# Kernel tuning notes

Measured on AMD Instinct MI355X. Metric: run time of the kernel, lower is better.

## Reference

```python
import jax, jax.numpy as jnp
import numpy as np

S = 2048        # q_len == context_length
HID = 4096      # hidden_size
NH = 32         # num_attention_heads
NKV = 8         # num_key_value_heads
HD = HID // NH  # head_dim = 128
THETA = 10000.0


def setup_inputs() -> dict:
    key = jax.random.key(0)
    ks = jax.random.split(key, 5)
    hidden_states = jax.random.normal(ks[0], (1, S, HID), dtype=jnp.float32)
    # 1x1 Conv2d weights == linear weights (out_ch, in_ch)
    wq = jax.random.normal(ks[1], (NH * HD, HID), dtype=jnp.float32) * 0.02
    wk = jax.random.normal(ks[2], (NKV * HD, HID), dtype=jnp.float32) * 0.02
    wv = jax.random.normal(ks[3], (NKV * HD, HID), dtype=jnp.float32) * 0.02
    wo = jax.random.normal(ks[4], (HID, NH * HD), dtype=jnp.float32) * 0.02
    # RoPE tables: rotate() only ever uses the first half_dim of cos/sin,
    # so build (1,1,S,half) directly (equivalent to cat(freqs,freqs) then slice).
    half = HD // 2
    inv_freq = 1.0 / (THETA ** (jnp.arange(0, HD, 2, dtype=jnp.float32) / HD))
    freqs = jnp.outer(jnp.arange(S, dtype=jnp.float32), inv_freq)  # (S, half)
    cos = jnp.cos(freqs)[None, None]  # (1,1,S,half)
    sin = jnp.sin(freqs)[None, None]
    # additive causal mask (1,1,S,S): 0 on/below diagonal, large negative above
    causal_mask = jnp.where(
        jnp.arange(S)[:, None] >= jnp.arange(S)[None, :], 0.0, -1e9
    ).astype(jnp.float32)[None, None]
    return dict(hidden_states=hidden_states, wq=wq, wk=wk, wv=wv, wo=wo,
                cos=cos, sin=sin, causal_mask=causal_mask)


def _rope(x, cos, sin):
    # x: (H, S, D); cos/sin: (1,1,S,D/2)
    half = x.shape[-1] // 2
    x1, x2 = x[..., :half], x[..., half:]
    c, s = cos[0, 0], sin[0, 0]  # (S, half), broadcasts over heads
    return jnp.concatenate([x1 * c - x2 * s, x2 * c + x1 * s], axis=-1)


def reference(hidden_states, wq, wk, wv, wo, cos, sin, causal_mask):
    x = hidden_states[0]               # (S, HID); bsz hard-coded to 1 in source
    seq = x.shape[0]
    # 1x1 conv projections == matmul; channel layout is head-major (h*HD + d)
    q = (x @ wq.T).reshape(seq, NH, HD).transpose(1, 0, 2)    # (NH, S, D)
    k = (x @ wk.T).reshape(seq, NKV, HD).transpose(1, 0, 2)   # (NKV, S, D)
    v = (x @ wv.T).reshape(seq, NKV, HD).transpose(1, 0, 2)   # (NKV, S, D)
    q = _rope(q, cos, sin)
    k = _rope(k, cos, sin)
    # repeat_kv: unsqueeze(1).repeat(n_rep).view -> head idx = rep*NKV + kv == tile
    n_rep = NH // NKV
    k = jnp.tile(k, (n_rep, 1, 1))     # (NH, S, D)
    v = jnp.tile(v, (n_rep, 1, 1))
    scale = 1.0 / np.sqrt(HD).astype(np.float32)
    scores = jnp.einsum('hqd,hkd->hqk', q, k) * scale + causal_mask[0, 0]
    attn = jax.nn.softmax(scores, axis=-1)                    # == ANE_softmax
    out = jnp.einsum('hqk,hkd->hqd', attn, v)                 # (NH, S, D)
    out = out.transpose(1, 0, 2).reshape(seq, NH * HD)        # (S, HID)
    return (out @ wo.T)[None]                                 # (1, S, HID)
```

## Files before the change

### kernel.cpp

```cpp
#include <hip/hip_runtime.h>
#include <hip/hip_bf16.h>

#define S_LEN 2048
#define HID   4096
#define NH    32
#define NKV   8
#define HD    128
#define QKV_N 6144
#define KDIM  4096

typedef __attribute__((ext_vector_type(8))) short short8;
typedef __attribute__((ext_vector_type(4))) float floatx4;
typedef unsigned short ushort;

__device__ __forceinline__ unsigned short f2bu(float f) {
  __hip_bfloat16 b = __float2bfloat16(f);
  return *reinterpret_cast<unsigned short*>(&b);
}
__device__ __forceinline__ void store_c(float* p, float v) { *p = v; }
__device__ __forceinline__ void store_c(__hip_bfloat16* p, float v) { *p = __float2bfloat16(v); }

__device__ __forceinline__ void async_copy16(const void* g, void* l) {
  __builtin_amdgcn_global_load_lds((const __attribute__((address_space(1))) void*)g,
                                   (__attribute__((address_space(3))) void*)l, 16, 0, 0);
}

struct bf16x4 { __hip_bfloat16 a, b, c, d; };
__global__ void cvt_f32_bf16(const float* __restrict__ src, __hip_bfloat16* __restrict__ dst, int n4) {
  int i = blockIdx.x * blockDim.x + threadIdx.x;
  if (i < n4) {
    float4 v = ((const float4*)src)[i];
    bf16x4 o = { __float2bfloat16(v.x), __float2bfloat16(v.y),
                 __float2bfloat16(v.z), __float2bfloat16(v.w) };
    ((bf16x4*)dst)[i] = o;
  }
}

template <typename CT>
__global__ __launch_bounds__(256, 2) void gemm_nt(const __hip_bfloat16* __restrict__ A,
                                                  const __hip_bfloat16* __restrict__ B,
                                                  CT* __restrict__ C, int M, int N, int K) {
  __shared__ __align__(16) ushort As[128 * 64];
  __shared__ __align__(16) ushort Bs[128 * 64];
  const int tid  = threadIdx.x;
  const int bm   = blockIdx.y * 128;
  const int bn   = blockIdx.x * 128;
  const int wave = tid >> 6;
  const int lane = tid & 63;
  const int ww   = (wave >> 1) * 64;
  const int wc   = (wave & 1) * 64;
  const int l15  = lane & 15;
  const int quad = lane >> 4;

  const ushort* Au = (const ushort*)A;
  const ushort* Bu = (const ushort*)B;

  const int rr  = lane >> 3;
  const int cc  = lane & 7;
  const int gch = cc ^ rr;
  const ushort* Ag = Au + (size_t)(bm + wave * 32 + rr) * K + gch * 8;
  const ushort* Bg = Bu + (size_t)(bn + wave * 32 + rr) * K + gch * 8;

  floatx4 acc[4][4] = {};

  for (int k0 = 0; k0 < K; k0 += 64) {
    __syncthreads();
#pragma unroll
    for (int e = 0; e < 4; ++e) {
      async_copy16(Ag + (size_t)(e * 8) * K + k0, &As[(wave * 32 + e * 8) * 64]);
      async_copy16(Bg + (size_t)(e * 8) * K + k0, &Bs[(wave * 32 + e * 8) * 64]);
    }
    __syncthreads();
#pragma unroll
    for (int kd = 0; kd < 2; ++kd) {
      short8 af[4], bf[4];
#pragma unroll
      for (int i = 0; i < 4; ++i) {
        af[i] = *(const short8*)&As[(ww + i * 16 + l15) * 64 + ((kd * 4 + quad) ^ (l15 & 7)) * 8];
        bf[i] = *(const short8*)&Bs[(wc + i * 16 + l15) * 64 + ((kd * 4 + quad) ^ (l15 & 7)) * 8];
      }
#pragma unroll
      for (int mi = 0; mi < 4; ++mi)
#pragma unroll
        for (int ni = 0; ni < 4; ++ni)
          acc[mi][ni] = __builtin_amdgcn_mfma_f32_16x16x32_bf16(af[mi], bf[ni], acc[mi][ni], 0, 0, 0);
    }
  }
#pragma unroll
  for (int mi = 0; mi < 4; ++mi)
#pragma unroll
    for (int ni = 0; ni < 4; ++ni)
#pragma unroll
      for (int r = 0; r < 4; ++r) {
        int row = bm + ww + mi * 16 + quad * 4 + r;
        int col = bn + wc + ni * 16 + l15;
        store_c(&C[(size_t)row * N + col], acc[mi][ni][r]);
      }
}

__global__ void rope_qk(const __hip_bfloat16* __restrict__ QKV,
                        const float* __restrict__ cosp, const float* __restrict__ sinp,
                        __hip_bfloat16* __restrict__ Qh, __hip_bfloat16* __restrict__ Kh) {
  int s = blockIdx.y;
  int col = blockIdx.x * 256 + threadIdx.x;
  if (col >= 5120) return;
  const size_t base = (size_t)s * QKV_N;
  float x = __bfloat162float(QKV[base + col]);
  int dd = col & 127;
  float val;
  if (dd < 64) {
    float xp = __bfloat162float(QKV[base + col + 64]);
    val = x * cosp[s * 64 + dd] - xp * sinp[s * 64 + dd];
  } else {
    int f = dd - 64;
    float xp = __bfloat162float(QKV[base + col - 64]);
    val = x * cosp[s * 64 + f] + xp * sinp[s * 64 + f];
  }
  if (col < HID) {
    int h = col >> 7;
    Qh[((size_t)h * S_LEN + s) * HD + dd] = __float2bfloat16(val * 0.08838834764831845f);
  } else {
    int h = (col - HID) >> 7;
    Kh[((size_t)h * S_LEN + s) * HD + dd] = __float2bfloat16(val);
  }
}

__global__ void v_transpose(const __hip_bfloat16* __restrict__ QKV, __hip_bfloat16* __restrict__ Vt) {
  __shared__ ushort tile[64][130];
  int h = blockIdx.y;
  int s0 = blockIdx.x * 64;
  int t = threadIdx.x;
  const ushort* src = (const ushort*)QKV;
#pragma unroll
  for (int i = 0; i < 32; ++i) {
    int flat = i * 256 + t;
    int r = flat >> 7, c = flat & 127;
    tile[r][c] = src[(size_t)(s0 + r) * QKV_N + 5120 + h * 128 + c];
  }
  __syncthreads();
  ushort* dst = (ushort*)Vt;
#pragma unroll
  for (int i = 0; i < 8; ++i) {
    int g = i * 256 + t;
    int d = g >> 4, j4 = (g & 15) * 4;
    ushort4 o;
    o.x = tile[j4][d]; o.y = tile[j4 + 1][d]; o.z = tile[j4 + 2][d]; o.w = tile[j4 + 3][d];
    *(ushort4*)&dst[((size_t)h * HD + d) * S_LEN + s0 + j4] = o;
  }
}

__global__ __launch_bounds__(256, 2) void attn(const __hip_bfloat16* __restrict__ Qh,
                                               const __hip_bfloat16* __restrict__ Kh,
                                               const __hip_bfloat16* __restrict__ Vt,
                                               __hip_bfloat16* __restrict__ AO) {
  __shared__ __align__(16) ushort Ks[2][64][128];
  __shared__ __align__(16) ushort P[4][32][72];
  const int bi   = blockIdx.x;
  const int head = bi & 31;
  const int slot = (bi >> 5) & 7;
  const int qt   = (bi >= 256) ? (2 * slot) : (15 - 2 * slot);
  const int wave = threadIdx.x >> 6;
  const int lane = threadIdx.x & 63;
  const int l15 = lane & 15, quad = lane >> 4;
  const int q0 = qt * 128 + wave * 32;
  const int hk = head & 7;
  const ushort* Qu = (const ushort*)Qh + (size_t)head * S_LEN * HD;
  const ushort* Ku = (const ushort*)Kh + (size_t)hk * S_LEN * HD;
  const ushort* Vu = (const ushort*)Vt + (size_t)hk * HD * S_LEN;

  const int rr4  = lane >> 4;
  const int cc16 = lane & 15;

  short8 qf[2][4];
#pragma unroll
  for (int mt = 0; mt < 2; ++mt)
#pragma unroll
    for (int kd = 0; kd < 4; ++kd)
      qf[mt][kd] = *(const short8*)(Qu + (size_t)(q0 + mt * 16 + l15) * HD + kd * 32 + quad * 8);

  floatx4 o[2][8] = {};
  float mst[2], lsum[2];
  mst[0] = mst[1] = -1e30f;
  lsum[0] = lsum[1] = 0.f;

  const int nsteps = 2 * (qt + 1);
  const int jendw = q0 + 32;

  auto stage = [&](int b, int j0) {
#pragma unroll
    for (int e = 0; e < 4; ++e) {
      int rt = e * 4 + rr4;
      int gc = cc16 ^ rt;
      async_copy16(Ku + (size_t)(j0 + wave * 16 + rt) * HD + gc * 8,
                   &Ks[b][wave * 16 + e * 4][0]);
    }
  };
  stage(0, 0);

  for (int s = 0; s < nsteps; ++s) {
    const int j0 = s * 64;
    __syncthreads();
    if (s + 1 < nsteps) stage((s + 1) & 1, (s + 1) * 64);
    if (j0 >= jendw) continue;
    const int b = s & 1;

    short8 vf0[8];
#pragma unroll
    for (int t = 0; t < 8; ++t)
      vf0[t] = *(const short8*)(Vu + (size_t)(t * 16 + l15) * S_LEN + j0 + quad * 8);

    floatx4 sc[2][4];
#pragma unroll
    for (int mt = 0; mt < 2; ++mt)
#pragma unroll
      for (int nt = 0; nt < 4; ++nt) sc[mt][nt] = floatx4{0.f, 0.f, 0.f, 0.f};
    __builtin_amdgcn_s_setprio(1);
#pragma unroll
    for (int nt = 0; nt < 4; ++nt) {
      short8 kf[4];
#pragma unroll
      for (int kd = 0; kd < 4; ++kd)
        kf[kd] = *(const short8*)&Ks[b][nt * 16 + l15][((kd * 4 + quad) ^ l15) * 8];
#pragma unroll
      for (int mt = 0; mt < 2; ++mt)
#pragma unroll
        for (int kd = 0; kd < 4; ++kd)
          sc[mt][nt] = __builtin_amdgcn_mfma_f32_16x16x32_bf16(kf[kd], qf[mt][kd], sc[mt][nt], 0, 0, 0);
    }
    __builtin_amdgcn_s_setprio(0);

    const bool domask = (j0 + 64 > q0);
#pragma unroll
    for (int mt = 0; mt < 2; ++mt) {
      const int qrow = q0 + mt * 16 + l15;
      float pv[16];
      float vm = -1e30f;
#pragma unroll
      for (int nt = 0; nt < 4; ++nt)
#pragma unroll
        for (int r = 0; r < 4; ++r) {
          float x = sc[mt][nt][r];
          if (domask && (j0 + nt * 16 + quad * 4 + r > qrow)) x = -1e30f;
          pv[nt * 4 + r] = x;
          vm = fmaxf(vm, x);
        }
      vm = fmaxf(vm, __shfl_xor(vm, 16));
      vm = fmaxf(vm, __shfl_xor(vm, 32));
      if (__any(vm > mst[mt] + 8.0f)) {
        const float mnew = fmaxf(mst[mt], vm);
        const float alpha = __expf(mst[mt] - mnew);
        mst[mt] = mnew;
        lsum[mt] *= alpha;
        float ar[4];
#pragma unroll
        for (int r = 0; r < 4; ++r)
          ar[r] = __shfl(alpha, (lane & 48) | (quad * 4 + r));
#pragma unroll
        for (int t = 0; t < 8; ++t)
#pragma unroll
          for (int r = 0; r < 4; ++r) o[mt][t][r] *= ar[r];
      }
      float ps = 0.f;
      ushort pk[16];
#pragma unroll
      for (int i = 0; i < 16; ++i) {
        float p = __expf(pv[i] - mst[mt]);
        ps += p;
        pk[i] = f2bu(p);
      }
      ps += __shfl_xor(ps, 16);
      ps += __shfl_xor(ps, 32);
      lsum[mt] += ps;
#pragma unroll
      for (int nt = 0; nt < 4; ++nt) {
        ushort4 w;
        w.x = pk[nt * 4 + 0]; w.y = pk[nt * 4 + 1];
        w.z = pk[nt * 4 + 2]; w.w = pk[nt * 4 + 3];
        *(ushort4*)&P[wave][mt * 16 + l15][nt * 16 + quad * 4] = w;
      }
    }

    short8 vf1[8];
#pragma unroll
    for (int t = 0; t < 8; ++t)
      vf1[t] = *(const short8*)(Vu + (size_t)(t * 16 + l15) * S_LEN + j0 + 32 + quad * 8);

    asm volatile("s_waitcnt lgkmcnt(0)" ::: "memory");
    short8 pf[2][2];
#pragma unroll
    for (int mt = 0; mt < 2; ++mt)
#pragma unroll
      for (int hh = 0; hh < 2; ++hh)
        pf[mt][hh] = *(const short8*)&P[wave][mt * 16 + l15][hh * 32 + quad * 8];
    __builtin_amdgcn_s_setprio(1);
#pragma unroll
    for (int t = 0; t < 8; ++t)
#pragma unroll
      for (int mt = 0; mt < 2; ++mt) {
        o[mt][t] = __builtin_amdgcn_mfma_f32_16x16x32_bf16(pf[mt][0], vf0[t], o[mt][t], 0, 0, 0);
        o[mt][t] = __builtin_amdgcn_mfma_f32_16x16x32_bf16(pf[mt][1], vf1[t], o[mt][t], 0, 0, 0);
      }
    __builtin_amdgcn_s_setprio(0);
  }

#pragma unroll
  for (int mt = 0; mt < 2; ++mt) {
    float inv[4];
#pragma unroll
    for (int r = 0; r < 4; ++r)
      inv[r] = 1.0f / __shfl(lsum[mt], (lane & 48) | (quad * 4 + r));
#pragma unroll
    for (int r = 0; r < 4; ++r) {
      const int row = q0 + mt * 16 + quad * 4 + r;
#pragma unroll
      for (int t = 0; t < 8; ++t)
        AO[(size_t)row * HID + head * HD + t * 16 + l15] = __float2bfloat16(o[mt][t][r] * inv[r]);
    }
  }
}

extern "C" void kernel_launch(void* const* d_in, const int* in_sizes, int n_in,
                              void* d_out, int out_size, void* d_ws, size_t ws_size,
                              hipStream_t stream) {
  const float* x    = (const float*)d_in[0];
  const float* wq   = (const float*)d_in[1];
  const float* wk   = (const float*)d_in[2];
  const float* wv   = (const float*)d_in[3];
  const float* wo   = (const float*)d_in[4];
  const float* cosp = (const float*)d_in[5];
  const float* sinp = (const float*)d_in[6];
  float* out = (float*)d_out;

  char* ws = (char*)d_ws;
  size_t off = 0;
  auto alloc = [&](size_t bytes) { char* p = ws + off; off += (bytes + 255) & ~255ull; return p; };
  __hip_bfloat16* Xb   = (__hip_bfloat16*)alloc((size_t)S_LEN * KDIM * 2);
  __hip_bfloat16* Wqkv = (__hip_bfloat16*)alloc((size_t)QKV_N * KDIM * 2);
  __hip_bfloat16* Wob  = (__hip_bfloat16*)alloc((size_t)HID * HID * 2);
  __hip_bfloat16* QKVb = (__hip_bfloat16*)alloc((size_t)S_LEN * QKV_N * 2);
  __hip_bfloat16* Qh   = (__hip_bfloat16*)alloc((size_t)NH * S_LEN * HD * 2);
  __hip_bfloat16* Kh   = (__hip_bfloat16*)alloc((size_t)NKV * S_LEN * HD * 2);
  __hip_bfloat16* Vt   = (__hip_bfloat16*)alloc((size_t)NKV * HD * S_LEN * 2);
  __hip_bfloat16* AO   = (__hip_bfloat16*)alloc((size_t)S_LEN * HID * 2);

  auto cvt = [&](const float* s, __hip_bfloat16* dpt, size_t n) {
    int n4 = (int)(n / 4);
    cvt_f32_bf16<<<dim3((n4 + 255) / 256), dim3(256), 0, stream>>>(s, dpt, n4);
  };
  cvt(x, Xb, (size_t)S_LEN * KDIM);
  cvt(wq, Wqkv, (size_t)HID * KDIM);
  cvt(wk, Wqkv + (size_t)HID * KDIM, (size_t)NKV * HD * KDIM);
  cvt(wv, Wqkv + (size_t)(HID + NKV * HD) * KDIM, (size_t)NKV * HD * KDIM);
  cvt(wo, Wob, (size_t)HID * HID);

  gemm_nt<__hip_bfloat16><<<dim3(QKV_N / 128, S_LEN / 128), dim3(256), 0, stream>>>(
      Xb, Wqkv, QKVb, S_LEN, QKV_N, KDIM);
  rope_qk<<<dim3(20, S_LEN), dim3(256), 0, stream>>>(QKVb, cosp, sinp, Qh, Kh);
  v_transpose<<<dim3(S_LEN / 64, NKV), dim3(256), 0, stream>>>(QKVb, Vt);
  attn<<<dim3(512), dim3(256), 0, stream>>>(Qh, Kh, Vt, AO);
  gemm_nt<float><<<dim3(HID / 128, S_LEN / 128), dim3(256), 0, stream>>>(
      AO, Wob, out, S_LEN, HID, KDIM);
}
```

Measured before the change: 551.7 us.

## Shrink attention q-tile to 64 rows and pair causal tiles per block

Each attention block now handles two 64-row query tiles (a late one and its mirror early one) with 16 rows per wave instead of one 128-row tile with 32 rows per wave. This balances causal work per block, drops the masked wasted K steps, and halves register and LDS use per wave, which may allow higher occupancy. It also chains K staging across the two tiles, defers the lsum reduction to the end, and computes exponentials speculatively before the rescale check. The trade-off is that each loaded K/V tile now feeds half as many query rows, so global and LDS traffic per FLOP increases.

```diff
diff --git a/kernel.cpp b/kernel.cpp
--- a/kernel.cpp
+++ b/kernel.cpp
@@ -154,15 +154,13 @@
                                                const __hip_bfloat16* __restrict__ Vt,
                                                __hip_bfloat16* __restrict__ AO) {
   __shared__ __align__(16) ushort Ks[2][64][128];
-  __shared__ __align__(16) ushort P[4][32][72];
+  __shared__ __align__(16) ushort P[4][16][72];
   const int bi   = blockIdx.x;
   const int head = bi & 31;
-  const int slot = (bi >> 5) & 7;
-  const int qt   = (bi >= 256) ? (2 * slot) : (15 - 2 * slot);
+  const int tp   = bi >> 5;
   const int wave = threadIdx.x >> 6;
   const int lane = threadIdx.x & 63;
   const int l15 = lane & 15, quad = lane >> 4;
-  const int q0 = qt * 128 + wave * 32;
   const int hk = head & 7;
   const ushort* Qu = (const ushort*)Qh + (size_t)head * S_LEN * HD;
   const ushort* Ku = (const ushort*)Kh + (size_t)hk * S_LEN * HD;
@@ -170,21 +168,6 @@
 
   const int rr4  = lane >> 4;
   const int cc16 = lane & 15;
-
-  short8 qf[2][4];
-#pragma unroll
-  for (int mt = 0; mt < 2; ++mt)
-#pragma unroll
-    for (int kd = 0; kd < 4; ++kd)
-      qf[mt][kd] = *(const short8*)(Qu + (size_t)(q0 + mt * 16 + l15) * HD + kd * 32 + quad * 8);
-
-  floatx4 o[2][8] = {};
-  float mst[2], lsum[2];
-  mst[0] = mst[1] = -1e30f;
-  lsum[0] = lsum[1] = 0.f;
-
-  const int nsteps = 2 * (qt + 1);
-  const int jendw = q0 + 32;
 
   auto stage = [&](int b, int j0) {
 #pragma unroll
@@ -195,126 +178,133 @@
                    &Ks[b][wave * 16 + e * 4][0]);
     }
   };
+
+  int gpar = 0;
   stage(0, 0);
 
-  for (int s = 0; s < nsteps; ++s) {
-    const int j0 = s * 64;
-    __syncthreads();
-    if (s + 1 < nsteps) stage((s + 1) & 1, (s + 1) * 64);
-    if (j0 >= jendw) continue;
-    const int b = s & 1;
-
-    short8 vf0[8];
-#pragma unroll
-    for (int t = 0; t < 8; ++t)
-      vf0[t] = *(const short8*)(Vu + (size_t)(t * 16 + l15) * S_LEN + j0 + quad * 8);
-
-    floatx4 sc[2][4];
-#pragma unroll
-    for (int mt = 0; mt < 2; ++mt)
-#pragma unroll
-      for (int nt = 0; nt < 4; ++nt) sc[mt][nt] = floatx4{0.f, 0.f, 0.f, 0.f};
-    __builtin_amdgcn_s_setprio(1);
-#pragma unroll
-    for (int nt = 0; nt < 4; ++nt) {
-      short8 kf[4];
-#pragma unroll
-      for (int kd = 0; kd < 4; ++kd)
-        kf[kd] = *(const short8*)&Ks[b][nt * 16 + l15][((kd * 4 + quad) ^ l15) * 8];
-#pragma unroll
-      for (int mt = 0; mt < 2; ++mt)
+  for (int ti = 0; ti < 2; ++ti) {
+    const int t = ti ? tp : (31 - tp);
+    const bool more = (ti == 0);
+    const int q0 = t * 64 + wave * 16;
+
+    short8 qf[4];
+#pragma unroll
+    for (int kd = 0; kd < 4; ++kd)
+      qf[kd] = *(const short8*)(Qu + (size_t)(q0 + l15) * HD + kd * 32 + quad * 8);
+
+    floatx4 o[8] = {};
+    float mst = -1e30f, lsum = 0.f;
+    const int nsteps = t + 1;
+
+    for (int s = 0; s < nsteps; ++s) {
+      const int j0 = s * 64;
+      __syncthreads();
+      if (s + 1 < nsteps)      stage((gpar + 1) & 1, (s + 1) * 64);
+      else if (more)           stage((gpar + 1) & 1, 0);
+      const int b = gpar & 1;
+      ++gpar;
+
+      short8 vf0[8];
+#pragma unroll
+      for (int t8 = 0; t8 < 8; ++t8)
+        vf0[t8] = *(const short8*)(Vu + (size_t)(t8 * 16 + l15) * S_LEN + j0 + quad * 8);
+
+      floatx4 sc[4] = {};
+      __builtin_amdgcn_s_setprio(1);
+#pragma unroll
+      for (int nt = 0; nt < 4; ++nt) {
+        short8 kf[4];
 #pragma unroll
         for (int kd = 0; kd < 4; ++kd)
-          sc[mt][nt] = __builtin_amdgcn_mfma_f32_16x16x32_bf16(kf[kd], qf[mt][kd], sc[mt][nt], 0, 0, 0);
-    }
-    __builtin_amdgcn_s_setprio(0);
-
-    const bool domask = (j0 + 64 > q0);
-#pragma unroll
-    for (int mt = 0; mt < 2; ++mt) {
-      const int qrow = q0 + mt * 16 + l15;
+          kf[kd] = *(const short8*)&Ks[b][nt * 16 + l15][((kd * 4 + quad) ^ l15) * 8];
+#pragma unroll
+        for (int kd = 0; kd < 4; ++kd)
+          sc[nt] = __builtin_amdgcn_mfma_f32_16x16x32_bf16(kf[kd], qf[kd], sc[nt], 0, 0, 0);
+      }
+      __builtin_amdgcn_s_setprio(0);
+
+      short8 vf1[8];
+#pragma unroll
+      for (int t8 = 0; t8 < 8; ++t8)
+        vf1[t8] = *(const short8*)(Vu + (size_t)(t8 * 16 + l15) * S_LEN + j0 + 32 + quad * 8);
+
+      const bool diag = (s == t);
       float pv[16];
-      float vm = -1e30f;
+      float vmloc = -1e30f;
 #pragma unroll
       for (int nt = 0; nt < 4; ++nt)
 #pragma unroll
         for (int r = 0; r < 4; ++r) {
-          float x = sc[mt][nt][r];
-          if (domask && (j0 + nt * 16 + quad * 4 + r > qrow)) x = -1e30f;
+          float x = sc[nt][r];
+          if (diag && (nt * 16 + quad * 4 + r > wave * 16 + l15)) x = -1e30f;
           pv[nt * 4 + r] = x;
-          vm = fmaxf(vm, x);
+          vmloc = fmaxf(vmloc, x);
         }
-      vm = fmaxf(vm, __shfl_xor(vm, 16));
+      float vm = fmaxf(vmloc, __shfl_xor(vmloc, 16));
       vm = fmaxf(vm, __shfl_xor(vm, 32));
-      if (__any(vm > mst[mt] + 8.0f)) {
-        const float mnew = fmaxf(mst[mt], vm);
-        const float alpha = __expf(mst[mt] - mnew);
-        mst[mt] = mnew;
-        lsum[mt] *= alpha;
-        float ar[4];
-#pragma unroll
-        for (int r = 0; r < 4; ++r)
-          ar[r] = __shfl(alpha, (lane & 48) | (quad * 4 + r));
-#pragma unroll
-        for (int t = 0; t < 8; ++t)
-#pragma unroll
-          for (int r = 0; r < 4; ++r) o[mt][t][r] *= ar[r];
-      }
       float ps = 0.f;
       ushort pk[16];
 #pragma unroll
       for (int i = 0; i < 16; ++i) {
-        float p = __expf(pv[i] - mst[mt]);
+        float p = __expf(pv[i] - mst);
         ps += p;
         pk[i] = f2bu(p);
       }
-      ps += __shfl_xor(ps, 16);
-      ps += __shfl_xor(ps, 32);
-      lsum[mt] += ps;
+      if (__any(vm > mst + 8.0f)) {
+        const float mnew = fmaxf(mst, vm);
+        const float al = __expf(mst - mnew);
+        mst = mnew;
+        lsum *= al;
+        ps = 0.f;
+#pragma unroll
+        for (int i = 0; i < 16; ++i) {
+          float p = __expf(pv[i] - mst);
+          ps += p;
+          pk[i] = f2bu(p);
+        }
+        float ar[4];
+#pragma unroll
+        for (int r = 0; r < 4; ++r)
+          ar[r] = __shfl(al, (lane & 48) | (quad * 4 + r));
+#pragma unroll
+        for (int t8 = 0; t8 < 8; ++t8)
+#pragma unroll
+          for (int r = 0; r < 4; ++r) o[t8][r] *= ar[r];
+      }
+      lsum += ps;
 #pragma unroll
       for (int nt = 0; nt < 4; ++nt) {
         ushort4 w;
         w.x = pk[nt * 4 + 0]; w.y = pk[nt * 4 + 1];
         w.z = pk[nt * 4 + 2]; w.w = pk[nt * 4 + 3];
-        *(ushort4*)&P[wave][mt * 16 + l15][nt * 16 + quad * 4] = w;
-      }
-    }
-
-    short8 vf1[8];
-#pragma unroll
-    for (int t = 0; t < 8; ++t)
-      vf1[t] = *(const short8*)(Vu + (size_t)(t * 16 + l15) * S_LEN + j0 + 32 + quad * 8);
-
-    asm volatile("s_waitcnt lgkmcnt(0)" ::: "memory");
-    short8 pf[2][2];
-#pragma unroll
-    for (int mt = 0; mt < 2; ++mt)
-#pragma unroll
-      for (int hh = 0; hh < 2; ++hh)
-        pf[mt][hh] = *(const short8*)&P[wave][mt * 16 + l15][hh * 32 + quad * 8];
-    __builtin_amdgcn_s_setprio(1);
-#pragma unroll
-    for (int t = 0; t < 8; ++t)
-#pragma unroll
-      for (int mt = 0; mt < 2; ++mt) {
-        o[mt][t] = __builtin_amdgcn_mfma_f32_16x16x32_bf16(pf[mt][0], vf0[t], o[mt][t], 0, 0, 0);
-        o[mt][t] = __builtin_amdgcn_mfma_f32_16x16x32_bf16(pf[mt][1], vf1[t], o[mt][t], 0, 0, 0);
-      }
-    __builtin_amdgcn_s_setprio(0);
-  }
-
-#pragma unroll
-  for (int mt = 0; mt < 2; ++mt) {
+        *(ushort4*)&P[wave][l15][nt * 16 + quad * 4] = w;
+      }
+
+      asm volatile("s_waitcnt lgkmcnt(0)" ::: "memory");
+      short8 pf0 = *(const short8*)&P[wave][l15][quad * 8];
+      short8 pf1 = *(const short8*)&P[wave][l15][32 + quad * 8];
+      __builtin_amdgcn_s_setprio(1);
+#pragma unroll
+      for (int t8 = 0; t8 < 8; ++t8)
+        o[t8] = __builtin_amdgcn_mfma_f32_16x16x32_bf16(pf0, vf0[t8], o[t8], 0, 0, 0);
+#pragma unroll
+      for (int t8 = 0; t8 < 8; ++t8)
+        o[t8] = __builtin_amdgcn_mfma_f32_16x16x32_bf16(pf1, vf1[t8], o[t8], 0, 0, 0);
+      __builtin_amdgcn_s_setprio(0);
+    }
+
+    lsum += __shfl_xor(lsum, 16);
+    lsum += __shfl_xor(lsum, 32);
     float inv[4];
 #pragma unroll
     for (int r = 0; r < 4; ++r)
-      inv[r] = 1.0f / __shfl(lsum[mt], (lane & 48) | (quad * 4 + r));
+      inv[r] = 1.0f / __shfl(lsum, (lane & 48) | (quad * 4 + r));
 #pragma unroll
     for (int r = 0; r < 4; ++r) {
-      const int row = q0 + mt * 16 + quad * 4 + r;
-#pragma unroll
-      for (int t = 0; t < 8; ++t)
-        AO[(size_t)row * HID + head * HD + t * 16 + l15] = __float2bfloat16(o[mt][t][r] * inv[r]);
+      const int row = q0 + quad * 4 + r;
+#pragma unroll
+      for (int t8 = 0; t8 < 8; ++t8)
+        AO[(size_t)row * HID + head * HD + t8 * 16 + l15] = __float2bfloat16(o[t8][r] * inv[r]);
     }
   }
 }
```

Measured after the change: 574.2 us. 1.04x slower.

## Split attention into 64-row q-tiles with two-wave blocks and single-buffered K

Applied to the files above, without the earlier changes.

Restructures the attention kernel so that each block runs 2 waves over a 64-row query tile, with 1024 blocks instead of 512. Blocks are ordered so long and short causal tiles interleave, which balances work across CUs. K staging moves to a single LDS buffer with an extra barrier, prefetched after the QK MFMAs. Softmax now exponentiates before the rescale check and recomputes only when the max jumps, and the row-sum reduction across lanes is deferred to the end. This cuts per-block imbalance and LDS use, but staging K now relies on a single buffer and one more sync per step.

```diff
diff --git a/kernel.cpp b/kernel.cpp
--- a/kernel.cpp
+++ b/kernel.cpp
@@ -149,27 +149,39 @@
   }
 }
 
-__global__ __launch_bounds__(256, 2) void attn(const __hip_bfloat16* __restrict__ Qh,
+__global__ __launch_bounds__(128, 2) void attn(const __hip_bfloat16* __restrict__ Qh,
                                                const __hip_bfloat16* __restrict__ Kh,
                                                const __hip_bfloat16* __restrict__ Vt,
                                                __hip_bfloat16* __restrict__ AO) {
-  __shared__ __align__(16) ushort Ks[2][64][128];
-  __shared__ __align__(16) ushort P[4][32][72];
+  __shared__ __align__(16) ushort Ks[64][128];
+  __shared__ __align__(16) ushort P[2][32][72];
   const int bi   = blockIdx.x;
-  const int head = bi & 31;
-  const int slot = (bi >> 5) & 7;
-  const int qt   = (bi >= 256) ? (2 * slot) : (15 - 2 * slot);
+  const int g    = bi >> 8;
+  const int c    = bi & 255;
+  const int head = c & 31;
+  const int u    = c >> 5;
+  const int t    = (g == 0) ? (24 + u) : (g == 1) ? (16 + u)
+                 : (g == 2) ? (15 - u) : (7 - u);
   const int wave = threadIdx.x >> 6;
   const int lane = threadIdx.x & 63;
   const int l15 = lane & 15, quad = lane >> 4;
-  const int q0 = qt * 128 + wave * 32;
   const int hk = head & 7;
+  const int q0 = t * 64 + wave * 32;
   const ushort* Qu = (const ushort*)Qh + (size_t)head * S_LEN * HD;
   const ushort* Ku = (const ushort*)Kh + (size_t)hk * S_LEN * HD;
   const ushort* Vu = (const ushort*)Vt + (size_t)hk * HD * S_LEN;
 
   const int rr4  = lane >> 4;
   const int cc16 = lane & 15;
+  auto stage = [&](int j0) {
+#pragma unroll
+    for (int e = 0; e < 8; ++e) {
+      int rt = (e * 4 + rr4) & 15;
+      int gc = cc16 ^ rt;
+      async_copy16(Ku + (size_t)(j0 + wave * 32 + e * 4 + rr4) * HD + gc * 8,
+                   &Ks[wave * 32 + e * 4][0]);
+    }
+  };
 
   short8 qf[2][4];
 #pragma unroll
@@ -182,32 +194,12 @@
   float mst[2], lsum[2];
   mst[0] = mst[1] = -1e30f;
   lsum[0] = lsum[1] = 0.f;
-
-  const int nsteps = 2 * (qt + 1);
-  const int jendw = q0 + 32;
-
-  auto stage = [&](int b, int j0) {
-#pragma unroll
-    for (int e = 0; e < 4; ++e) {
-      int rt = e * 4 + rr4;
-      int gc = cc16 ^ rt;
-      async_copy16(Ku + (size_t)(j0 + wave * 16 + rt) * HD + gc * 8,
-                   &Ks[b][wave * 16 + e * 4][0]);
-    }
-  };
-  stage(0, 0);
-
+  const int nsteps = t + 1;
+
+  stage(0);
   for (int s = 0; s < nsteps; ++s) {
     const int j0 = s * 64;
     __syncthreads();
-    if (s + 1 < nsteps) stage((s + 1) & 1, (s + 1) * 64);
-    if (j0 >= jendw) continue;
-    const int b = s & 1;
-
-    short8 vf0[8];
-#pragma unroll
-    for (int t = 0; t < 8; ++t)
-      vf0[t] = *(const short8*)(Vu + (size_t)(t * 16 + l15) * S_LEN + j0 + quad * 8);
 
     floatx4 sc[2][4];
 #pragma unroll
@@ -220,7 +212,7 @@
       short8 kf[4];
 #pragma unroll
       for (int kd = 0; kd < 4; ++kd)
-        kf[kd] = *(const short8*)&Ks[b][nt * 16 + l15][((kd * 4 + quad) ^ l15) * 8];
+        kf[kd] = *(const short8*)&Ks[nt * 16 + l15][((kd * 4 + quad) ^ l15) * 8];
 #pragma unroll
       for (int mt = 0; mt < 2; ++mt)
 #pragma unroll
@@ -228,38 +220,31 @@
           sc[mt][nt] = __builtin_amdgcn_mfma_f32_16x16x32_bf16(kf[kd], qf[mt][kd], sc[mt][nt], 0, 0, 0);
     }
     __builtin_amdgcn_s_setprio(0);
-
-    const bool domask = (j0 + 64 > q0);
+    __syncthreads();
+    if (s + 1 < nsteps) stage(j0 + 64);
+
+    short8 vf0[8];
+#pragma unroll
+    for (int t8 = 0; t8 < 8; ++t8)
+      vf0[t8] = *(const short8*)(Vu + (size_t)(t8 * 16 + l15) * S_LEN + j0 + quad * 8);
+
+    const bool diag = (s == t);
 #pragma unroll
     for (int mt = 0; mt < 2; ++mt) {
-      const int qrow = q0 + mt * 16 + l15;
+      const int qloc = wave * 32 + mt * 16 + l15;
       float pv[16];
-      float vm = -1e30f;
+      float vmloc = -1e30f;
 #pragma unroll
       for (int nt = 0; nt < 4; ++nt)
 #pragma unroll
         for (int r = 0; r < 4; ++r) {
           float x = sc[mt][nt][r];
-          if (domask && (j0 + nt * 16 + quad * 4 + r > qrow)) x = -1e30f;
+          if (diag && (nt * 16 + quad * 4 + r > qloc)) x = -1e30f;
           pv[nt * 4 + r] = x;
-          vm = fmaxf(vm, x);
+          vmloc = fmaxf(vmloc, x);
         }
-      vm = fmaxf(vm, __shfl_xor(vm, 16));
+      float vm = fmaxf(vmloc, __shfl_xor(vmloc, 16));
       vm = fmaxf(vm, __shfl_xor(vm, 32));
-      if (__any(vm > mst[mt] + 8.0f)) {
-        const float mnew = fmaxf(mst[mt], vm);
-        const float alpha = __expf(mst[mt] - mnew);
-        mst[mt] = mnew;
-        lsum[mt] *= alpha;
-        float ar[4];
-#pragma unroll
-        for (int r = 0; r < 4; ++r)
-          ar[r] = __shfl(alpha, (lane & 48) | (quad * 4 + r));
-#pragma unroll
-        for (int t = 0; t < 8; ++t)
-#pragma unroll
-          for (int r = 0; r < 4; ++r) o[mt][t][r] *= ar[r];
-      }
       float ps = 0.f;
       ushort pk[16];
 #pragma unroll
@@ -268,8 +253,27 @@
         ps += p;
         pk[i] = f2bu(p);
       }
-      ps += __shfl_xor(ps, 16);
-      ps += __shfl_xor(ps, 32);
+      if (__any(vm > mst[mt] + 8.0f)) {
+        const float mnew = fmaxf(mst[mt], vm);
+        const float al = __expf(mst[mt] - mnew);
+        mst[mt] = mnew;
+        lsum[mt] *= al;
+        ps = 0.f;
+#pragma unroll
+        for (int i = 0; i < 16; ++i) {
+          float p = __expf(pv[i] - mst[mt]);
+          ps += p;
+          pk[i] = f2bu(p);
+        }
+        float ar[4];
+#pragma unroll
+        for (int r = 0; r < 4; ++r)
+          ar[r] = __shfl(al, (lane & 48) | (quad * 4 + r));
+#pragma unroll
+        for (int t8 = 0; t8 < 8; ++t8)
+#pragma unroll
+          for (int r = 0; r < 4; ++r) o[mt][t8][r] *= ar[r];
+      }
       lsum[mt] += ps;
 #pragma unroll
       for (int nt = 0; nt < 4; ++nt) {
@@ -282,8 +286,8 @@
 
     short8 vf1[8];
 #pragma unroll
-    for (int t = 0; t < 8; ++t)
-      vf1[t] = *(const short8*)(Vu + (size_t)(t * 16 + l15) * S_LEN + j0 + 32 + quad * 8);
+    for (int t8 = 0; t8 < 8; ++t8)
+      vf1[t8] = *(const short8*)(Vu + (size_t)(t8 * 16 + l15) * S_LEN + j0 + 32 + quad * 8);
 
     asm volatile("s_waitcnt lgkmcnt(0)" ::: "memory");
     short8 pf[2][2];
@@ -294,27 +298,30 @@
         pf[mt][hh] = *(const short8*)&P[wave][mt * 16 + l15][hh * 32 + quad * 8];
     __builtin_amdgcn_s_setprio(1);
 #pragma unroll
-    for (int t = 0; t < 8; ++t)
+    for (int t8 = 0; t8 < 8; ++t8)
 #pragma unroll
       for (int mt = 0; mt < 2; ++mt) {
-        o[mt][t] = __builtin_amdgcn_mfma_f32_16x16x32_bf16(pf[mt][0], vf0[t], o[mt][t], 0, 0, 0);
-        o[mt][t] = __builtin_amdgcn_mfma_f32_16x16x32_bf16(pf[mt][1], vf1[t], o[mt][t], 0, 0, 0);
+        o[mt][t8] = __builtin_amdgcn_mfma_f32_16x16x32_bf16(pf[mt][0], vf0[t8], o[mt][t8], 0, 0, 0);
+        o[mt][t8] = __builtin_amdgcn_mfma_f32_16x16x32_bf16(pf[mt][1], vf1[t8], o[mt][t8], 0, 0, 0);
       }
     __builtin_amdgcn_s_setprio(0);
   }
 
 #pragma unroll
   for (int mt = 0; mt < 2; ++mt) {
+    float ls = lsum[mt];
+    ls += __shfl_xor(ls, 16);
+    ls += __shfl_xor(ls, 32);
     float inv[4];
 #pragma unroll
     for (int r = 0; r < 4; ++r)
-      inv[r] = 1.0f / __shfl(lsum[mt], (lane & 48) | (quad * 4 + r));
+      inv[r] = 1.0f / __shfl(ls, (lane & 48) | (quad * 4 + r));
 #pragma unroll
     for (int r = 0; r < 4; ++r) {
       const int row = q0 + mt * 16 + quad * 4 + r;
 #pragma unroll
-      for (int t = 0; t < 8; ++t)
-        AO[(size_t)row * HID + head * HD + t * 16 + l15] = __float2bfloat16(o[mt][t][r] * inv[r]);
+      for (int t8 = 0; t8 < 8; ++t8)
+        AO[(size_t)row * HID + head * HD + t8 * 16 + l15] = __float2bfloat16(o[mt][t8][r] * inv[r]);
     }
   }
 }
@@ -357,7 +364,7 @@
       Xb, Wqkv, QKVb, S_LEN, QKV_N, KDIM);
   rope_qk<<<dim3(20, S_LEN), dim3(256), 0, stream>>>(QKVb, cosp, sinp, Qh, Kh);
   v_transpose<<<dim3(S_LEN / 64, NKV), dim3(256), 0, stream>>>(QKVb, Vt);
-  attn<<<dim3(512), dim3(256), 0, stream>>>(Qh, Kh, Vt, AO);
+  attn<<<dim3(1024), dim3(128), 0, stream>>>(Qh, Kh, Vt, AO);
   gemm_nt<float><<<dim3(HID / 128, S_LEN / 128), dim3(256), 0, stream>>>(
       AO, Wob, out, S_LEN, HID, KDIM);
 }
```

After: 529.7 us. -4.0%, faster.
